# Kernel optimization log

Hardware: AMD Instinct MI355X
Metric: run time of the kernel (lower is better)

Reference implementation:

```python
import jax, jax.numpy as jnp
import numpy as np
from jax import lax

IN_CH = 512
OUT_CH = 512
K = 3
W_DIM = 512
PAD = K // 2
EPS = 1e-8


def setup_inputs() -> dict:
    key = jax.random.key(0)
    k1, k2, k3, k4 = jax.random.split(key, 4)
    B, H, W = 8, 64, 64
    x = jax.random.normal(k1, (B, IN_CH, H, W), dtype=jnp.float32)
    w = jax.random.normal(k2, (B, W_DIM), dtype=jnp.float32)
    weight = jax.random.normal(k3, (OUT_CH, IN_CH, K, K), dtype=jnp.float32)
    bias = jnp.zeros((OUT_CH,), dtype=jnp.float32)
    # nn.Linear(512, in_ch): weight [in_ch, 512], bias [in_ch]
    lim = 1.0 / np.sqrt(W_DIM)
    affine_w = jax.random.uniform(k4, (IN_CH, W_DIM), dtype=jnp.float32, minval=-lim, maxval=lim)
    affine_b = jnp.zeros((IN_CH,), dtype=jnp.float32)
    return {"x": x, "w": w, "weight": weight, "bias": bias,
            "affine_w": affine_w, "affine_b": affine_b}


def _conv_one(xi, wi):
    # xi: [C, H, W], wi: [O, C, K, K] -> [O, H, W]
    out = lax.conv_general_dilated(
        xi[None], wi, window_strides=(1, 1),
        padding=[(PAD, PAD), (PAD, PAD)],
        dimension_numbers=("NCHW", "OIHW", "NCHW"))
    return out[0]


def reference(x, w, weight, bias, affine_w, affine_b):
    # style: [B, C] -> broadcast as [B, 1, C, 1, 1]
    style = w @ affine_w.T + affine_b
    wmod = weight[None] * (style[:, None, :, None, None] + 1.0)  # [B, O, C, K, K]
    # demodulate
    sigma = lax.rsqrt(jnp.sum(wmod * wmod, axis=(2, 3, 4), keepdims=True) + EPS)
    wmod = wmod * sigma
    # per-sample conv (equivalent to groups=B grouped conv)
    out = jax.vmap(_conv_one)(x, wmod)  # [B, O, H, W]
    return out + bias[None, :, None, None]
```

## Files before the change

### kernel.cpp

```cpp
#include <hip/hip_runtime.h>
#include <hip/hip_bf16.h>

typedef __attribute__((ext_vector_type(8))) short bf16x8;
typedef __attribute__((ext_vector_type(4))) float f32x4;

#define FSW(c) (((c) >> 1) & 3)

static __device__ __forceinline__ uint bf16rne(float f) {
    uint u = __float_as_uint(f);
    return (u + 0x7fffu + ((u >> 16) & 1u)) >> 16;
}

__global__ void k_prep1(const float* __restrict__ weight, ushort* __restrict__ Wf,
                        float* __restrict__ wsq, const float* __restrict__ w,
                        const float* __restrict__ aw, const float* __restrict__ ab,
                        float* __restrict__ style) {
    if (blockIdx.x < 1024) {
        int t = blockIdx.x * 256 + threadIdx.x;
        int o = t >> 9, c = t & 511;
        int grp = o >> 5, rr = o & 31, fm = rr >> 4, l15r = rr & 15;
        int chunkid = c >> 5, kgw = (c >> 3) & 3, kk = c & 7;
        int lanew = kgw * 16 + l15r;
        const float* wp = weight + (size_t)t * 9;
        size_t G = (size_t)(grp * 16 + chunkid);
        size_t base = G * 9216 + (size_t)fm * 512 + (size_t)lanew * 8 + kk;
        float sq = 0.f;
        #pragma unroll
        for (int j = 0; j < 9; ++j) {
            float v = wp[j];
            sq += v * v;
            Wf[base + (size_t)j * 1024] = (ushort)bf16rne(v);
        }
        wsq[t] = sq;
    } else {
        int idx = (blockIdx.x - 1024) * 4 + (threadIdx.x >> 6);
        int lane = threadIdx.x & 63;
        int b = idx >> 9, c = idx & 511;
        const float* wp = w + b * 512;
        const float* ap = aw + (size_t)c * 512;
        float s = 0.f;
        #pragma unroll
        for (int i = 0; i < 8; ++i) s += wp[lane + i * 64] * ap[lane + i * 64];
        #pragma unroll
        for (int m = 32; m; m >>= 1) s += __shfl_xor(s, m, 64);
        if (lane == 0) style[idx] = s + ab[c] + 1.0f;
    }
}

__global__ void k_prep2(const float* __restrict__ style, const float* __restrict__ wsq,
                        float* __restrict__ sigma, const float* __restrict__ x,
                        ushort* __restrict__ xb) {
    if (blockIdx.x < 1024) {
        int idx = blockIdx.x * 4 + (threadIdx.x >> 6);
        int lane = threadIdx.x & 63;
        int b = idx >> 9, o = idx & 511;
        const float* sp = style + b * 512;
        const float* qp = wsq + (size_t)o * 512;
        float s = 0.f;
        #pragma unroll
        for (int i = 0; i < 8; ++i) {
            float st = sp[lane + i * 64];
            s += st * st * qp[lane + i * 64];
        }
        #pragma unroll
        for (int m = 32; m; m >>= 1) s += __shfl_xor(s, m, 64);
        if (lane == 0) sigma[idx] = rsqrtf(s + 1e-8f);
    } else {
        int bid = blockIdx.x - 1024;
        int b = bid >> 6, y = bid & 63;
        int xcol = threadIdx.x >> 2, cg = threadIdx.x & 3;
        const float* sp = style + b * 512;
        #pragma unroll 1
        for (int cb = 0; cb < 16; ++cb) {
            int c0 = cb * 32 + cg * 8;
            float v[8];
            #pragma unroll
            for (int j = 0; j < 8; ++j)
                v[j] = x[((size_t)(b * 512 + c0 + j) * 64 + y) * 64 + xcol] * sp[c0 + j];
            uint4 pk;
            pk.x = bf16rne(v[0]) | (bf16rne(v[1]) << 16);
            pk.y = bf16rne(v[2]) | (bf16rne(v[3]) << 16);
            pk.z = bf16rne(v[4]) | (bf16rne(v[5]) << 16);
            pk.w = bf16rne(v[6]) | (bf16rne(v[7]) << 16);
            *(uint4*)&xb[((size_t)(b * 64 + y) * 64 + xcol) * 512 + c0] = pk;
        }
    }
}

#define ALOAD(SL, DY, CC) { \
    _Pragma("unroll") for (int dx_ = 0; dx_ < 3; ++dx_) \
    _Pragma("unroll") for (int fm_ = 0; fm_ < 4; ++fm_) \
        SL[dx_ * 4 + fm_] = *(const uint4*)((fm_ < 2 ? Wbase0 : Wbase1) \
            + (size_t)(CC) * 9216 + ((DY) * 3 + dx_) * 1024 + (fm_ & 1) * 512); }

#define HGROUP(AARR, H) \
    _Pragma("unroll") for (int dx_ = 0; dx_ < 3; ++dx_) \
    _Pragma("unroll") for (int q_ = 0; q_ < 2; ++q_) \
    _Pragma("unroll") for (int fm_ = 0; fm_ < 4; ++fm_) \
        acc[fm_][(H) * 2 + q_] = __builtin_amdgcn_mfma_f32_16x16x32_bf16( \
            *(const bf16x8*)&AARR[dx_ * 4 + fm_], bv[dx_ * 2 + q_], \
            acc[fm_][(H) * 2 + q_], 0, 0, 0);

#define ROW(R, MFMAS) { \
    bf16x8 bv[6]; \
    _Pragma("unroll") for (int dx_ = 0; dx_ < 3; ++dx_) \
    _Pragma("unroll") for (int q_ = 0; q_ < 2; ++q_) { \
        int ci_ = dx_ + cb32 + q_ * 16 + l15; \
        bv[dx_ * 2 + q_] = *(const bf16x8*)&sX[cur][((R) * 66 + ci_) * 32 + ((kg ^ FSW(ci_)) * 8)]; \
    } \
    __builtin_amdgcn_s_setprio(1); \
    MFMAS \
    __builtin_amdgcn_s_setprio(0); }

#define XLOAD(CC) { \
    _Pragma("unroll") for (int p_ = 0; p_ < 4; ++p_) { \
        int yy_ = y0 - 1 + p_; \
        xs[p_] = ((unsigned)yy_ < 64u) \
               ? *(const uint4*)(xrow_base + (size_t)yy_ * 32768 + (CC) * 32) \
               : make_uint4(0u, 0u, 0u, 0u); \
    } }

#define XWRITE(BUF) { \
    _Pragma("unroll") for (int p_ = 0; p_ < 4; ++p_) \
        *(uint4*)&sX[BUF][(p_ * 66 + colpos) * 32 + sslot] = xs[p_]; }

#define CHUNK(CCI, NCC, A0_, A1_) { \
    XLOAD(NCC) \
    ROW(0, HGROUP(A0_, 0)) \
    ROW(1, HGROUP(A0_, 1) HGROUP(A1_, 0)) \
    ALOAD(A0_, 2, CCI)             \
    ROW(2, HGROUP(A1_, 1) HGROUP(A0_, 0)) \
    ALOAD(A1_, 0, NCC)             \
    ROW(3, HGROUP(A0_, 1)) \
    XWRITE(cur ^ 1) \
    __syncthreads(); \
    cur ^= 1; \
    ALOAD(A0_, 1, NCC)             \
}

__global__ __launch_bounds__(256, 2) void k_conv(
    const ushort* __restrict__ xb, const ushort* __restrict__ Wf,
    const float* __restrict__ sigma, const float* __restrict__ bias,
    float* __restrict__ out) {

    __shared__ ushort sX[2][4 * 66 * 32];

    const int tid = threadIdx.x, bid = blockIdx.x;
    const int ob = bid >> 8;
    const int pb = ((bid & 7) << 5) | ((bid >> 3) & 31);
    const int b = pb >> 5, y0 = (pb & 31) * 2;
    const int o0 = ob * 128;
    const int wv = tid >> 6, lane = tid & 63;
    const int l15 = lane & 15, kg = lane >> 4;
    const int wr = wv >> 1;
    const int cb32 = (wv & 1) * 32;

    const int scol = (tid >> 2) & 63;
    const int skg = tid & 3;
    const int colpos = scol + 1;
    const int sslot = (skg ^ FSW(colpos)) * 8;
    const ushort* xrow_base = xb + ((size_t)(b * 64) * 64 + scol) * 512 + skg * 8;

    const ushort* Wbase0 = Wf + (size_t)(ob * 4 + wr * 2) * 147456 + lane * 8;
    const ushort* Wbase1 = Wbase0 + 147456;

    f32x4 acc[4][4];
    #pragma unroll
    for (int i = 0; i < 4; ++i)
        #pragma unroll
        for (int j = 0; j < 4; ++j) acc[i][j] = (f32x4){0.f, 0.f, 0.f, 0.f};

    if (tid < 64) {
        int buf = tid >> 5, rem = tid & 31;
        int r = rem >> 3, side = (rem >> 2) & 1, sl = rem & 3;
        int cp = side * 65;
        *(uint4*)&sX[buf][(r * 66 + cp) * 32 + sl * 8] = make_uint4(0u, 0u, 0u, 0u);
    }

    uint4 xs[4];
    XLOAD(0)
    XWRITE(0)

    uint4 aX[12], aY[12];
    ALOAD(aX, 0, 0) ALOAD(aY, 1, 0)
    __syncthreads();

    int cur = 0;
    #pragma unroll 1
    for (int it = 0; it < 8; ++it) {
        const int c0 = it * 2, c1 = it * 2 + 1, c2 = (it * 2 + 2) & 15;
        CHUNK(c0, c1, aX, aY)
        CHUNK(c1, c2, aY, aX)
    }

    const float* sigb = sigma + b * 512;
    #pragma unroll
    for (int fm = 0; fm < 4; ++fm) {
        #pragma unroll
        for (int j = 0; j < 4; ++j) {
            int o = o0 + wr * 64 + fm * 16 + kg * 4 + j;
            float sg = sigb[o];
            float bs = bias[o];
            float* op = out + ((size_t)(b * 512 + o) * 64 + y0) * 64;
            #pragma unroll
            for (int h = 0; h < 2; ++h)
                #pragma unroll
                for (int q = 0; q < 2; ++q)
                    op[h * 64 + cb32 + q * 16 + l15] = acc[fm][h * 2 + q][j] * sg + bs;
        }
    }
}

extern "C" void kernel_launch(void* const* d_in, const int* in_sizes, int n_in,
                              void* d_out, int out_size, void* d_ws, size_t ws_size,
                              hipStream_t stream) {
    const float* x    = (const float*)d_in[0];
    const float* w    = (const float*)d_in[1];
    const float* wt   = (const float*)d_in[2];
    const float* bias = (const float*)d_in[3];
    const float* aw   = (const float*)d_in[4];
    const float* ab   = (const float*)d_in[5];
    float* out = (float*)d_out;

    float* style  = (float*)d_ws;
    float* sigmap = style + 4096;
    float* wsq    = sigmap + 4096;
    ushort* Wf    = (ushort*)(wsq + 512 * 512);
    ushort* xbm   = Wf + 2359296;

    k_prep1<<<2048, 256, 0, stream>>>(wt, Wf, wsq, w, aw, ab, style);
    k_prep2<<<1536, 256, 0, stream>>>(style, wsq, sigmap, x, xbm);
    k_conv <<<1024, 256, 0, stream>>>(xbm, Wf, sigmap, bias, out);
}
```

Before: 152.2 us.

## Split conv work across 8 waves and stage input tiles via global_load_lds

The conv kernel moves from 4 waves per block, each computing 64 output channels, to 8 waves each computing 32 channels. This halves the accumulator and weight-register footprint per wave and raises occupancy. The input tile is now copied straight into LDS with global_load_lds instead of going through registers and an explicit LDS write. A new zeroing path handles the out-of-range border rows. The trade-off is that each wave reuses fewer weights, so more wavefronts issue weight loads and LDS B-operand reads.

```diff
diff --git a/kernel.cpp b/kernel.cpp
--- a/kernel.cpp
+++ b/kernel.cpp
@@ -5,6 +5,13 @@
 typedef __attribute__((ext_vector_type(4))) float f32x4;
 
 #define FSW(c) (((c) >> 1) & 3)
+
+typedef __attribute__((address_space(3))) unsigned int lds_uint;
+typedef const __attribute__((address_space(1))) unsigned int gl_uint;
+
+static __device__ __forceinline__ void gll16(const ushort* g, ushort* l) {
+    __builtin_amdgcn_global_load_lds((gl_uint*)g, (lds_uint*)l, 16, 0, 0);
+}
 
 static __device__ __forceinline__ uint bf16rne(float f) {
     uint u = __float_as_uint(f);
@@ -88,57 +95,51 @@
 }
 
 #define ALOAD(SL, DY, CC) { \
-    _Pragma("unroll") for (int dx_ = 0; dx_ < 3; ++dx_) \
-    _Pragma("unroll") for (int fm_ = 0; fm_ < 4; ++fm_) \
-        SL[dx_ * 4 + fm_] = *(const uint4*)((fm_ < 2 ? Wbase0 : Wbase1) \
-            + (size_t)(CC) * 9216 + ((DY) * 3 + dx_) * 1024 + (fm_ & 1) * 512); }
+    const ushort* p_ = Wbase + (size_t)(CC) * 9216 + (DY) * 3072; \
+    _Pragma("unroll") for (int q_ = 0; q_ < 6; ++q_) \
+        SL[q_] = *(const uint4*)(p_ + q_ * 512); }
 
 #define HGROUP(AARR, H) \
     _Pragma("unroll") for (int dx_ = 0; dx_ < 3; ++dx_) \
     _Pragma("unroll") for (int q_ = 0; q_ < 2; ++q_) \
-    _Pragma("unroll") for (int fm_ = 0; fm_ < 4; ++fm_) \
+    _Pragma("unroll") for (int fm_ = 0; fm_ < 2; ++fm_) \
         acc[fm_][(H) * 2 + q_] = __builtin_amdgcn_mfma_f32_16x16x32_bf16( \
-            *(const bf16x8*)&AARR[dx_ * 4 + fm_], bv[dx_ * 2 + q_], \
+            *(const bf16x8*)&AARR[dx_ * 2 + fm_], bv[dx_ * 2 + q_], \
             acc[fm_][(H) * 2 + q_], 0, 0, 0);
 
 #define ROW(R, MFMAS) { \
     bf16x8 bv[6]; \
     _Pragma("unroll") for (int dx_ = 0; dx_ < 3; ++dx_) \
     _Pragma("unroll") for (int q_ = 0; q_ < 2; ++q_) { \
-        int ci_ = dx_ + cb32 + q_ * 16 + l15; \
+        int ci_ = dx_ + ch * 32 + q_ * 16 + l15; \
         bv[dx_ * 2 + q_] = *(const bf16x8*)&sX[cur][((R) * 66 + ci_) * 32 + ((kg ^ FSW(ci_)) * 8)]; \
     } \
     __builtin_amdgcn_s_setprio(1); \
     MFMAS \
     __builtin_amdgcn_s_setprio(0); }
 
-#define XLOAD(CC) { \
-    _Pragma("unroll") for (int p_ = 0; p_ < 4; ++p_) { \
-        int yy_ = y0 - 1 + p_; \
-        xs[p_] = ((unsigned)yy_ < 64u) \
-               ? *(const uint4*)(xrow_base + (size_t)yy_ * 32768 + (CC) * 32) \
-               : make_uint4(0u, 0u, 0u, 0u); \
+#define XSTAGE(BUF, CC) { \
+    if (yok) { \
+        gll16(src0 + (size_t)yy * 32768 + (CC) * 32, \
+              &sX[BUF][(srow * 66 + ch * 16 + 1) * 32]); \
+        gll16(src1 + (size_t)yy * 32768 + (CC) * 32, \
+              &sX[BUF][(srow * 66 + (ch + 2) * 16 + 1) * 32]); \
     } }
 
-#define XWRITE(BUF) { \
-    _Pragma("unroll") for (int p_ = 0; p_ < 4; ++p_) \
-        *(uint4*)&sX[BUF][(p_ * 66 + colpos) * 32 + sslot] = xs[p_]; }
-
 #define CHUNK(CCI, NCC, A0_, A1_) { \
-    XLOAD(NCC) \
+    XSTAGE(cur ^ 1, NCC) \
     ROW(0, HGROUP(A0_, 0)) \
     ROW(1, HGROUP(A0_, 1) HGROUP(A1_, 0)) \
     ALOAD(A0_, 2, CCI)             \
     ROW(2, HGROUP(A1_, 1) HGROUP(A0_, 0)) \
     ALOAD(A1_, 0, NCC)             \
     ROW(3, HGROUP(A0_, 1)) \
-    XWRITE(cur ^ 1) \
     __syncthreads(); \
     cur ^= 1; \
     ALOAD(A0_, 1, NCC)             \
 }
 
-__global__ __launch_bounds__(256, 2) void k_conv(
+__global__ __launch_bounds__(512, 4) void k_conv(
     const ushort* __restrict__ xb, const ushort* __restrict__ Wf,
     const float* __restrict__ sigma, const float* __restrict__ bias,
     float* __restrict__ out) {
@@ -152,21 +153,26 @@
     const int o0 = ob * 128;
     const int wv = tid >> 6, lane = tid & 63;
     const int l15 = lane & 15, kg = lane >> 4;
-    const int wr = wv >> 1;
-    const int cb32 = (wv & 1) * 32;
-
-    const int scol = (tid >> 2) & 63;
-    const int skg = tid & 3;
-    const int colpos = scol + 1;
-    const int sslot = (skg ^ FSW(colpos)) * 8;
-    const ushort* xrow_base = xb + ((size_t)(b * 64) * 64 + scol) * 512 + skg * 8;
-
-    const ushort* Wbase0 = Wf + (size_t)(ob * 4 + wr * 2) * 147456 + lane * 8;
-    const ushort* Wbase1 = Wbase0 + 147456;
-
-    f32x4 acc[4][4];
+    const int og = wv >> 1;
+    const int ch = wv & 1;
+
+    const int srow = og;
+    const int yy = y0 - 1 + srow;
+    const bool yok = (unsigned)yy < 64u;
+    const int c0col = ch * 16 + (lane >> 2);
+    const int c1col = (ch + 2) * 16 + (lane >> 2);
+    const int skg = lane & 3;
+    const ushort* src0 = xb + ((size_t)(b * 64) * 64 + c0col) * 512
+                       + (size_t)((skg ^ FSW(c0col + 1)) * 8);
+    const ushort* src1 = xb + ((size_t)(b * 64) * 64 + c1col) * 512
+                       + (size_t)((skg ^ FSW(c1col + 1)) * 8);
+
+    const int grp = ob * 4 + og;
+    const ushort* Wbase = Wf + (size_t)grp * 147456 + lane * 8;
+
+    f32x4 acc[2][4];
     #pragma unroll
-    for (int i = 0; i < 4; ++i)
+    for (int i = 0; i < 2; ++i)
         #pragma unroll
         for (int j = 0; j < 4; ++j) acc[i][j] = (f32x4){0.f, 0.f, 0.f, 0.f};
 
@@ -176,12 +182,17 @@
         int cp = side * 65;
         *(uint4*)&sX[buf][(r * 66 + cp) * 32 + sl * 8] = make_uint4(0u, 0u, 0u, 0u);
     }
-
-    uint4 xs[4];
-    XLOAD(0)
-    XWRITE(0)
-
-    uint4 aX[12], aY[12];
+    if (y0 == 0 || y0 == 62) {
+        const int r = (y0 == 0) ? 0 : 3;
+        #pragma unroll 1
+        for (int i = tid; i < 528; i += 512) {
+            int buf = i >= 264, j = (i >= 264) ? i - 264 : i;
+            *(uint4*)&sX[buf][(r * 66 + (j >> 2)) * 32 + (j & 3) * 8] = make_uint4(0u, 0u, 0u, 0u);
+        }
+    }
+
+    XSTAGE(0, 0)
+    uint4 aX[6], aY[6];
     ALOAD(aX, 0, 0) ALOAD(aY, 1, 0)
     __syncthreads();
 
@@ -195,18 +206,18 @@
 
     const float* sigb = sigma + b * 512;
     #pragma unroll
-    for (int fm = 0; fm < 4; ++fm) {
+    for (int fm = 0; fm < 2; ++fm) {
         #pragma unroll
         for (int j = 0; j < 4; ++j) {
-            int o = o0 + wr * 64 + fm * 16 + kg * 4 + j;
+            int o = o0 + og * 32 + fm * 16 + kg * 4 + j;
             float sg = sigb[o];
             float bs = bias[o];
-            float* op = out + ((size_t)(b * 512 + o) * 64 + y0) * 64;
+            float* op = out + ((size_t)(b * 512 + o) * 64 + y0) * 64 + ch * 32;
             #pragma unroll
             for (int h = 0; h < 2; ++h)
                 #pragma unroll
                 for (int q = 0; q < 2; ++q)
-                    op[h * 64 + cb32 + q * 16 + l15] = acc[fm][h * 2 + q][j] * sg + bs;
+                    op[h * 64 + q * 16 + l15] = acc[fm][h * 2 + q][j] * sg + bs;
         }
     }
 }
@@ -230,5 +241,5 @@
 
     k_prep1<<<2048, 256, 0, stream>>>(wt, Wf, wsq, w, aw, ab, style);
     k_prep2<<<1536, 256, 0, stream>>>(style, wsq, sigmap, x, xbm);
-    k_conv <<<1024, 256, 0, stream>>>(xbm, Wf, sigmap, bias, out);
-}
+    k_conv <<<1024, 512, 0, stream>>>(xbm, Wf, sigmap, bias, out);
+}
```

Result: slower. 158.5 us (+4.1%).
